# Optimization experiments

Measured on AMD Instinct MI355X. Metric: run time of the kernel, lower is better.

## Reference

```python
import jax, jax.numpy as jnp
import numpy as np

A_VOCAB = 400000   # embedding table rows (a)
D = 200            # embedding_dim, hard-coded as 200 in the original module
C = 50000          # number of concepts
T = 1000000        # total flattened ancestor entries (~20 per concept)
B = 1024           # batch of input vectors x


def setup_inputs() -> dict:
    key = jax.random.key(0)
    k1, k2, k3, k4 = jax.random.split(key, 4)
    return {
        "x": jax.random.normal(k1, (B, D), dtype=jnp.float32),
        "embed_weight": jax.random.normal(k2, (A_VOCAB, D), dtype=jnp.float32) * 0.02,
        "ancestor_ids": jax.random.randint(k3, (T,), 0, A_VOCAB, dtype=jnp.int32),
        "segment_ids": jnp.sort(jax.random.randint(k4, (T,), 0, C, dtype=jnp.int32)),
        "n_concepts": C,
    }


def reference(x, embed_weight, ancestor_ids, segment_ids, n_concepts):
    # Ragged gather + per-concept sum (the original's Python loop over concepts)
    gathered = embed_weight[ancestor_ids]                                   # [T, D]
    local_H = jax.ops.segment_sum(gathered, segment_ids,
                                  num_segments=n_concepts)                  # [C, D]
    # concept_vector = local_H @ x.T ; output = softmax(concept_vector.T, dim=1)
    logits = jnp.einsum('bd,cd->bc', x, local_H)                            # [B, C]
    return jax.nn.softmax(logits, axis=1)
```

## Files before the change

### kernel.cpp

```cpp
#include <hip/hip_runtime.h>
#include <hip/hip_bf16.h>

#define DDIM   200
#define CSEG   50000
#define TTOT   1000000
#define BROWS  1024
#define KPAD   224
#define NTILE  64
#define NT     782
#define NPAD   50048
#define MTILES 8
#define GEMM_BLOCKS (NT * MTILES)

typedef __attribute__((ext_vector_type(8))) __bf16 bf16x8;
typedef __attribute__((ext_vector_type(4))) float  f32x4;
typedef unsigned short u16;

#define WS_XB    0
#define WS_HB    458752
#define WS_PART  (458752 + 22421504)
#define WS_INV   (458752 + 22421504 + 3203072)
#define WS_START (458752 + 22421504 + 3203072 + 4096)

__device__ inline u16 f2bf(float f) {
  unsigned u = __float_as_uint(f);
  u += 0x7FFFu + ((u >> 16) & 1u);
  return (u16)(u >> 16);
}

__global__ __launch_bounds__(256) void fused_prep_kernel(const int* __restrict__ sid,
                                                         int* __restrict__ start,
                                                         const float* __restrict__ x,
                                                         u16* __restrict__ xb) {
  const int gtid = blockIdx.x * 256 + threadIdx.x;
  if (gtid < TTOT) {
    const int cur = sid[gtid];
    const int prev = (gtid == 0) ? -1 : sid[gtid - 1];
    for (int c = prev + 1; c <= cur; ++c) start[c] = gtid;
    if (gtid == TTOT - 1) {
      for (int c = cur + 1; c <= CSEG; ++c) start[c] = TTOT;
    }
  }
  if (gtid < BROWS * 56) {
    const int row = gtid / 56;
    const int col = (gtid % 56) * 4;
    ushort4 o = make_ushort4(0, 0, 0, 0);
    if (col < DDIM) {
      const float4 v = *reinterpret_cast<const float4*>(x + (size_t)row * DDIM + col);
      o = make_ushort4(f2bf(v.x), f2bf(v.y), f2bf(v.z), f2bf(v.w));
    }
    *reinterpret_cast<ushort4*>(xb + (size_t)row * KPAD + col) = o;
  }
}

__global__ __launch_bounds__(256) void seg_sum_kernel(const float* __restrict__ embed,
                                                      const int* __restrict__ aid,
                                                      const int* __restrict__ start,
                                                      u16* __restrict__ Hb) {
  const int wave = threadIdx.x >> 6;
  const int lane = threadIdx.x & 63;
  const int c = blockIdx.x * 4 + wave;
  if (c >= NPAD || lane >= 56) return;
  const int col = lane * 4;
  const bool act = (col < DDIM);
  float4 a[8];
#pragma unroll
  for (int j = 0; j < 8; ++j) a[j] = make_float4(0.f, 0.f, 0.f, 0.f);
  if (c < CSEG && act) {
    const int s = start[c], e = start[c + 1];
    for (int t = s; t < e; t += 8) {
      int   idx[8];
      float msk[8];
#pragma unroll
      for (int j = 0; j < 8; ++j) {
        const int tt = t + j;
        const bool ok = (tt < e);
        idx[j] = aid[ok ? tt : s];
        msk[j] = ok ? 1.f : 0.f;
      }
#pragma unroll
      for (int j = 0; j < 8; ++j) {
        const float4 v = *reinterpret_cast<const float4*>(
            embed + (size_t)idx[j] * DDIM + col);
        a[j].x = fmaf(msk[j], v.x, a[j].x);
        a[j].y = fmaf(msk[j], v.y, a[j].y);
        a[j].z = fmaf(msk[j], v.z, a[j].z);
        a[j].w = fmaf(msk[j], v.w, a[j].w);
      }
    }
#pragma unroll
    for (int j = 4; j < 8; ++j) {
      a[j - 4].x += a[j].x; a[j - 4].y += a[j].y;
      a[j - 4].z += a[j].z; a[j - 4].w += a[j].w;
    }
    a[0].x += a[1].x + a[2].x + a[3].x;
    a[0].y += a[1].y + a[2].y + a[3].y;
    a[0].z += a[1].z + a[2].z + a[3].z;
    a[0].w += a[1].w + a[2].w + a[3].w;
  }
  const ushort4 o = (c < CSEG && act)
      ? make_ushort4(f2bf(a[0].x), f2bf(a[0].y), f2bf(a[0].z), f2bf(a[0].w))
      : make_ushort4(0, 0, 0, 0);
  *reinterpret_cast<ushort4*>(Hb + (size_t)c * KPAD + col) = o;
}

__device__ inline void gemm_block_map(int orig, int* ntile, int* mtile) {
  const int f = (orig & 7) * (GEMM_BLOCKS / 8) + (orig >> 3);
  *ntile = f >> 3;
  *mtile = f & 7;
}

__device__ inline void gemm_tile(const u16* __restrict__ xb, const u16* __restrict__ Hb,
                                 int m0, int n0, int lane, f32x4 acc[2][4]) {
  const int r  = lane & 15;
  const int ko = (lane >> 4) * 8;
  const u16* xp = xb + (size_t)(m0 + r) * KPAD + ko;
  const u16* hp = Hb + (size_t)(n0 + r) * KPAD + ko;
  for (int ks = 0; ks < KPAD / 32; ++ks) {
    const int kb = ks * 32;
    const bf16x8 a0 = *reinterpret_cast<const bf16x8*>(xp + kb);
    const bf16x8 a1 = *reinterpret_cast<const bf16x8*>(xp + 16 * KPAD + kb);
#pragma unroll
    for (int ni = 0; ni < 4; ++ni) {
      const bf16x8 b = *reinterpret_cast<const bf16x8*>(hp + (size_t)ni * 16 * KPAD + kb);
      acc[0][ni] = __builtin_amdgcn_mfma_f32_16x16x32_bf16(a0, b, acc[0][ni], 0, 0, 0);
      acc[1][ni] = __builtin_amdgcn_mfma_f32_16x16x32_bf16(a1, b, acc[1][ni], 0, 0, 0);
    }
  }
}

__global__ __launch_bounds__(256) void gemm_pass1_kernel(const u16* __restrict__ xb,
                                                         const u16* __restrict__ Hb,
                                                         float* __restrict__ partials) {
  int ntile, mtile;
  gemm_block_map(blockIdx.x, &ntile, &mtile);
  const int lane = threadIdx.x & 63, wave = threadIdx.x >> 6;
  const int m0 = mtile * 128 + wave * 32;
  const int n0 = ntile * NTILE;
  f32x4 acc[2][4] = {};
  gemm_tile(xb, Hb, m0, n0, lane, acc);
  const int cbase = n0 + (lane & 15);
#pragma unroll
  for (int mi = 0; mi < 2; ++mi) {
#pragma unroll
    for (int rr = 0; rr < 4; ++rr) {
      float s = 0.f;
#pragma unroll
      for (int ni = 0; ni < 4; ++ni) {
        if (cbase + ni * 16 < CSEG) s += __expf(acc[mi][ni][rr]);
      }
      for (int off = 1; off < 16; off <<= 1) s += __shfl_xor(s, off, 64);
      if ((lane & 15) == 0) {
        const int row = m0 + mi * 16 + (lane >> 4) * 4 + rr;
        partials[(size_t)row * NT + ntile] = s;
      }
    }
  }
}

__global__ __launch_bounds__(256) void reduce_kernel(const float* __restrict__ partials,
                                                     float* __restrict__ invs) {
  const int row = blockIdx.x, tid = threadIdx.x;
  float s = 0.f;
  for (int nt = tid; nt < NT; nt += 256) s += partials[(size_t)row * NT + nt];
  __shared__ float sm[256];
  sm[tid] = s;
  __syncthreads();
  for (int st = 128; st > 0; st >>= 1) {
    if (tid < st) sm[tid] += sm[tid + st];
    __syncthreads();
  }
  if (tid == 0) invs[row] = 1.0f / sm[0];
}

__global__ __launch_bounds__(256) void gemm_pass2_kernel(const u16* __restrict__ xb,
                                                         const u16* __restrict__ Hb,
                                                         const float* __restrict__ invs,
                                                         float* __restrict__ out) {
  int ntile, mtile;
  gemm_block_map(blockIdx.x, &ntile, &mtile);
  const int lane = threadIdx.x & 63, wave = threadIdx.x >> 6;
  const int m0 = mtile * 128 + wave * 32;
  const int n0 = ntile * NTILE;
  f32x4 acc[2][4] = {};
  gemm_tile(xb, Hb, m0, n0, lane, acc);
  const int c0 = n0 + (lane & 15);
#pragma unroll
  for (int mi = 0; mi < 2; ++mi) {
#pragma unroll
    for (int rr = 0; rr < 4; ++rr) {
      const int row = m0 + mi * 16 + (lane >> 4) * 4 + rr;
      const float inv = invs[row];
      float* orow = out + (size_t)row * CSEG;
#pragma unroll
      for (int ni = 0; ni < 4; ++ni) {
        const int col = c0 + ni * 16;
        if (col < CSEG) {
          __builtin_nontemporal_store(__expf(acc[mi][ni][rr]) * inv, &orow[col]);
        }
      }
    }
  }
}

extern "C" void kernel_launch(void* const* d_in, const int* in_sizes, int n_in,
                              void* d_out, int out_size, void* d_ws, size_t ws_size,
                              hipStream_t stream) {
  const float* x     = (const float*)d_in[0];
  const float* embed = (const float*)d_in[1];
  const int*   aid   = (const int*)d_in[2];
  const int*   sid   = (const int*)d_in[3];

  char* ws = (char*)d_ws;
  u16*   xb       = (u16*)(ws + WS_XB);
  u16*   Hb       = (u16*)(ws + WS_HB);
  float* partials = (float*)(ws + WS_PART);
  float* invs     = (float*)(ws + WS_INV);
  int*   start    = (int*)(ws + WS_START);
  float* out      = (float*)d_out;

  hipLaunchKernelGGL(fused_prep_kernel, dim3((TTOT + 255) / 256), dim3(256), 0, stream,
                     sid, start, x, xb);
  hipLaunchKernelGGL(seg_sum_kernel,    dim3(NPAD / 4),    dim3(256), 0, stream,
                     embed, aid, start, Hb);
  hipLaunchKernelGGL(gemm_pass1_kernel, dim3(GEMM_BLOCKS), dim3(256), 0, stream,
                     xb, Hb, partials);
  hipLaunchKernelGGL(reduce_kernel,     dim3(BROWS),       dim3(256), 0, stream,
                     partials, invs);
  hipLaunchKernelGGL(gemm_pass2_kernel, dim3(GEMM_BLOCKS), dim3(256), 0, stream,
                     xb, Hb, invs, out);
}
```

Baseline: 318.5 us.

## Gather from a bf16 copy of the embedding table and stage H tiles in LDS

Adds a pass that converts the whole fp32 embedding table to bf16 in workspace, then gathers from it in the segment sum, halving the bytes moved by the random row gather. The bf16 path runs only when the workspace is large enough to hold the converted table. Each call must now stream the full table (read fp32, write bf16), which may cost as much as the gather saves. The GEMM passes also preload A fragments into registers and stage the 64-row H tile in padded LDS, so the four waves share one global load of H.

```diff
diff --git a/kernel.cpp b/kernel.cpp
--- a/kernel.cpp
+++ b/kernel.cpp
@@ -11,21 +11,29 @@
 #define NPAD   50048
 #define MTILES 8
 #define GEMM_BLOCKS (NT * MTILES)
+#define LDSROW 232
 
 typedef __attribute__((ext_vector_type(8))) __bf16 bf16x8;
 typedef __attribute__((ext_vector_type(4))) float  f32x4;
 typedef unsigned short u16;
-
-#define WS_XB    0
-#define WS_HB    458752
-#define WS_PART  (458752 + 22421504)
-#define WS_INV   (458752 + 22421504 + 3203072)
-#define WS_START (458752 + 22421504 + 3203072 + 4096)
+typedef __attribute__((ext_vector_type(8))) unsigned short u16x8;
+typedef __attribute__((ext_vector_type(4))) unsigned short u16x4;
+
+#define WS_XB    0u
+#define WS_HB    458752u
+#define WS_PART  (WS_HB + 22421504u)
+#define WS_INV   (WS_PART + 3203072u)
+#define WS_START (WS_INV + 4096u)
+#define WS_EBF   (WS_START + 200704u)
+#define WS_TOTAL_BF16 ((size_t)WS_EBF + 160000000u)
 
 __device__ inline u16 f2bf(float f) {
   unsigned u = __float_as_uint(f);
   u += 0x7FFFu + ((u >> 16) & 1u);
   return (u16)(u >> 16);
+}
+__device__ inline float bf2f(u16 h) {
+  return __uint_as_float(((unsigned)h) << 16);
 }
 
 __global__ __launch_bounds__(256) void fused_prep_kernel(const int* __restrict__ sid,
@@ -53,6 +61,69 @@
   }
 }
 
+__global__ __launch_bounds__(256) void conv_embed_kernel(const float* __restrict__ embed,
+                                                         u16* __restrict__ ebf) {
+  const long long n4 = (long long)400000 * DDIM / 4;
+  const long long stride = (long long)gridDim.x * 256;
+  for (long long i = (long long)blockIdx.x * 256 + threadIdx.x; i < n4; i += stride) {
+    const f32x4 v = __builtin_nontemporal_load(reinterpret_cast<const f32x4*>(embed) + i);
+    u16x4 o;
+    o.x = f2bf(v.x); o.y = f2bf(v.y); o.z = f2bf(v.z); o.w = f2bf(v.w);
+    *(reinterpret_cast<u16x4*>(ebf) + i) = o;
+  }
+}
+
+__global__ __launch_bounds__(256) void seg_sum_bf16_kernel(const u16* __restrict__ ebf,
+                                                           const int* __restrict__ aid,
+                                                           const int* __restrict__ start,
+                                                           u16* __restrict__ Hb) {
+  const int wave = threadIdx.x >> 6;
+  const int lane = threadIdx.x & 63;
+  const int c = blockIdx.x * 4 + wave;
+  if (c >= NPAD || lane >= 56) return;
+  const int col = lane * 4;
+  const bool act = (col < DDIM);
+  float4 a[8];
+#pragma unroll
+  for (int j = 0; j < 8; ++j) a[j] = make_float4(0.f, 0.f, 0.f, 0.f);
+  if (c < CSEG && act) {
+    const int s = start[c], e = start[c + 1];
+    for (int t = s; t < e; t += 8) {
+      int   idx[8];
+      float msk[8];
+#pragma unroll
+      for (int j = 0; j < 8; ++j) {
+        const int tt = t + j;
+        const bool ok = (tt < e);
+        idx[j] = aid[ok ? tt : s];
+        msk[j] = ok ? 1.f : 0.f;
+      }
+#pragma unroll
+      for (int j = 0; j < 8; ++j) {
+        const ushort4 v = *reinterpret_cast<const ushort4*>(
+            ebf + (size_t)idx[j] * DDIM + col);
+        a[j].x = fmaf(msk[j], bf2f(v.x), a[j].x);
+        a[j].y = fmaf(msk[j], bf2f(v.y), a[j].y);
+        a[j].z = fmaf(msk[j], bf2f(v.z), a[j].z);
+        a[j].w = fmaf(msk[j], bf2f(v.w), a[j].w);
+      }
+    }
+#pragma unroll
+    for (int j = 4; j < 8; ++j) {
+      a[j - 4].x += a[j].x; a[j - 4].y += a[j].y;
+      a[j - 4].z += a[j].z; a[j - 4].w += a[j].w;
+    }
+    a[0].x += a[1].x + a[2].x + a[3].x;
+    a[0].y += a[1].y + a[2].y + a[3].y;
+    a[0].z += a[1].z + a[2].z + a[3].z;
+    a[0].w += a[1].w + a[2].w + a[3].w;
+  }
+  const ushort4 o = (c < CSEG && act)
+      ? make_ushort4(f2bf(a[0].x), f2bf(a[0].y), f2bf(a[0].z), f2bf(a[0].w))
+      : make_ushort4(0, 0, 0, 0);
+  *reinterpret_cast<ushort4*>(Hb + (size_t)c * KPAD + col) = o;
+}
+
 __global__ __launch_bounds__(256) void seg_sum_kernel(const float* __restrict__ embed,
                                                       const int* __restrict__ aid,
                                                       const int* __restrict__ start,
@@ -110,21 +181,37 @@
   *mtile = f & 7;
 }
 
-__device__ inline void gemm_tile(const u16* __restrict__ xb, const u16* __restrict__ Hb,
-                                 int m0, int n0, int lane, f32x4 acc[2][4]) {
+__device__ inline void gemm_tile_lds(const u16* __restrict__ xb,
+                                     const u16* __restrict__ Hb,
+                                     u16* hlds, int m0, int n0, int tid,
+                                     f32x4 acc[2][4]) {
+  const int lane = tid & 63;
   const int r  = lane & 15;
   const int ko = (lane >> 4) * 8;
   const u16* xp = xb + (size_t)(m0 + r) * KPAD + ko;
-  const u16* hp = Hb + (size_t)(n0 + r) * KPAD + ko;
-  for (int ks = 0; ks < KPAD / 32; ++ks) {
-    const int kb = ks * 32;
-    const bf16x8 a0 = *reinterpret_cast<const bf16x8*>(xp + kb);
-    const bf16x8 a1 = *reinterpret_cast<const bf16x8*>(xp + 16 * KPAD + kb);
+  bf16x8 afrag[7][2];
+#pragma unroll
+  for (int ks = 0; ks < 7; ++ks) {
+    afrag[ks][0] = *reinterpret_cast<const bf16x8*>(xp + ks * 32);
+    afrag[ks][1] = *reinterpret_cast<const bf16x8*>(xp + 16 * KPAD + ks * 32);
+  }
+#pragma unroll
+  for (int k = 0; k < 7; ++k) {
+    const int i = tid + k * 256;
+    const int row = i / 28, c8 = i % 28;
+    const u16x8 h = *reinterpret_cast<const u16x8*>(
+        Hb + (size_t)(n0 + row) * KPAD + c8 * 8);
+    *reinterpret_cast<u16x8*>(hlds + row * LDSROW + c8 * 8) = h;
+  }
+  __syncthreads();
+#pragma unroll
+  for (int ks = 0; ks < 7; ++ks) {
 #pragma unroll
     for (int ni = 0; ni < 4; ++ni) {
-      const bf16x8 b = *reinterpret_cast<const bf16x8*>(hp + (size_t)ni * 16 * KPAD + kb);
-      acc[0][ni] = __builtin_amdgcn_mfma_f32_16x16x32_bf16(a0, b, acc[0][ni], 0, 0, 0);
-      acc[1][ni] = __builtin_amdgcn_mfma_f32_16x16x32_bf16(a1, b, acc[1][ni], 0, 0, 0);
+      const bf16x8 b = *reinterpret_cast<const bf16x8*>(
+          hlds + (r + ni * 16) * LDSROW + ko + ks * 32);
+      acc[0][ni] = __builtin_amdgcn_mfma_f32_16x16x32_bf16(afrag[ks][0], b, acc[0][ni], 0, 0, 0);
+      acc[1][ni] = __builtin_amdgcn_mfma_f32_16x16x32_bf16(afrag[ks][1], b, acc[1][ni], 0, 0, 0);
     }
   }
 }
@@ -132,13 +219,14 @@
 __global__ __launch_bounds__(256) void gemm_pass1_kernel(const u16* __restrict__ xb,
                                                          const u16* __restrict__ Hb,
                                                          float* __restrict__ partials) {
+  __shared__ u16 hlds[64 * LDSROW];
   int ntile, mtile;
   gemm_block_map(blockIdx.x, &ntile, &mtile);
   const int lane = threadIdx.x & 63, wave = threadIdx.x >> 6;
   const int m0 = mtile * 128 + wave * 32;
   const int n0 = ntile * NTILE;
   f32x4 acc[2][4] = {};
-  gemm_tile(xb, Hb, m0, n0, lane, acc);
+  gemm_tile_lds(xb, Hb, hlds, m0, n0, threadIdx.x, acc);
   const int cbase = n0 + (lane & 15);
 #pragma unroll
   for (int mi = 0; mi < 2; ++mi) {
@@ -177,13 +265,14 @@
                                                          const u16* __restrict__ Hb,
                                                          const float* __restrict__ invs,
                                                          float* __restrict__ out) {
+  __shared__ u16 hlds[64 * LDSROW];
   int ntile, mtile;
   gemm_block_map(blockIdx.x, &ntile, &mtile);
   const int lane = threadIdx.x & 63, wave = threadIdx.x >> 6;
   const int m0 = mtile * 128 + wave * 32;
   const int n0 = ntile * NTILE;
   f32x4 acc[2][4] = {};
-  gemm_tile(xb, Hb, m0, n0, lane, acc);
+  gemm_tile_lds(xb, Hb, hlds, m0, n0, threadIdx.x, acc);
   const int c0 = n0 + (lane & 15);
 #pragma unroll
   for (int mi = 0; mi < 2; ++mi) {
@@ -217,12 +306,21 @@
   float* partials = (float*)(ws + WS_PART);
   float* invs     = (float*)(ws + WS_INV);
   int*   start    = (int*)(ws + WS_START);
+  u16*   ebf      = (u16*)(ws + WS_EBF);
   float* out      = (float*)d_out;
+
+  const bool use_bf16 = (ws_size >= WS_TOTAL_BF16);
 
   hipLaunchKernelGGL(fused_prep_kernel, dim3((TTOT + 255) / 256), dim3(256), 0, stream,
                      sid, start, x, xb);
-  hipLaunchKernelGGL(seg_sum_kernel,    dim3(NPAD / 4),    dim3(256), 0, stream,
-                     embed, aid, start, Hb);
+  if (use_bf16) {
+    hipLaunchKernelGGL(conv_embed_kernel, dim3(2048), dim3(256), 0, stream, embed, ebf);
+    hipLaunchKernelGGL(seg_sum_bf16_kernel, dim3(NPAD / 4), dim3(256), 0, stream,
+                       ebf, aid, start, Hb);
+  } else {
+    hipLaunchKernelGGL(seg_sum_kernel, dim3(NPAD / 4), dim3(256), 0, stream,
+                       embed, aid, start, Hb);
+  }
   hipLaunchKernelGGL(gemm_pass1_kernel, dim3(GEMM_BLOCKS), dim3(256), 0, stream,
                      xb, Hb, partials);
   hipLaunchKernelGGL(reduce_kernel,     dim3(BROWS),       dim3(256), 0, stream,
```

New measurement: 273.3 us. 1.17x faster.
